# Optimization experiments

Hardware: AMD Instinct MI355X
Metric: run time of the kernel (lower is better)

The kernel has to match this reference:

```python
import jax, jax.numpy as jnp
import numpy as np

B, N, D, S, ITERS = 64, 2048, 256, 8, 3
SCALE = D ** -0.5
EPS_LN = 1e-5

def _ln(x, g, b):
    m = jnp.mean(x, axis=-1, keepdims=True)
    v = jnp.var(x, axis=-1, keepdims=True)
    return (x - m) / jnp.sqrt(v + EPS_LN) * g + b

def setup_inputs() -> dict:
    key = jax.random.key(0)
    ks = jax.random.split(key, 20)
    s = D ** -0.5
    f32 = jnp.float32
    return dict(
        x=jax.random.normal(ks[0], (B, N, D), f32),
        noise=jax.random.normal(ks[1], (B, S, D), f32),
        slots_mu=jax.random.normal(ks[2], (1, 1, D), f32),
        slots_sigma=jax.random.normal(ks[3], (1, 1, D), f32),
        Wq=jax.random.normal(ks[4], (D, D), f32) * s, bq=jnp.zeros((D,), f32),
        Wk=jax.random.normal(ks[5], (D, D), f32) * s, bk=jnp.zeros((D,), f32),
        Wv=jax.random.normal(ks[6], (D, D), f32) * s, bv=jnp.zeros((D,), f32),
        W_ih=jax.random.normal(ks[7], (3 * D, D), f32) * s, b_ih=jnp.zeros((3 * D,), f32),
        W_hh=jax.random.normal(ks[8], (3 * D, D), f32) * s, b_hh=jnp.zeros((3 * D,), f32),
        W1=jax.random.normal(ks[9], (D, D), f32) * s, b1=jnp.zeros((D,), f32),
        W2=jax.random.normal(ks[10], (D, D), f32) * s, b2=jnp.zeros((D,), f32),
        g_in=jnp.ones((D,), f32), be_in=jnp.zeros((D,), f32),
        g_sl=jnp.ones((D,), f32), be_sl=jnp.zeros((D,), f32),
        g_ff=jnp.ones((D,), f32), be_ff=jnp.zeros((D,), f32),
    )

def reference(x, noise, slots_mu, slots_sigma, Wq, bq, Wk, bk, Wv, bv,
              W_ih, b_ih, W_hh, b_hh, W1, b1, W2, b2,
              g_in, be_in, g_sl, be_sl, g_ff, be_ff):
    # slot init: mu + softplus(sigma) * noise  -> [B,S,D]
    slots = slots_mu + jax.nn.softplus(slots_sigma) * noise
    xn = _ln(x, g_in, be_in)
    k = xn @ Wk.T + bk  # [B,N,D]
    v = xn @ Wv.T + bv
    for _ in range(ITERS):
        prev = slots
        q = _ln(slots, g_sl, be_sl) @ Wq.T + bq  # [B,S,D]
        logits = jnp.einsum('bsd,bnd->bsn', q, k) * SCALE
        attn = jax.nn.softmax(logits, axis=-1) + 1e-8  # softmax over inputs, as in source
        attn = attn / jnp.sum(attn, axis=-1, keepdims=True)
        updates = jnp.einsum('bsn,bnd->bsd', attn, v)
        # GRUCell(input=updates, hidden=prev); torch gate order r,z,n
        gi = updates @ W_ih.T + b_ih
        gh = prev @ W_hh.T + b_hh
        ir, iz, i_n = jnp.split(gi, 3, axis=-1)
        hr, hz, h_n = jnp.split(gh, 3, axis=-1)
        r = jax.nn.sigmoid(ir + hr)
        z = jax.nn.sigmoid(iz + hz)
        n = jnp.tanh(i_n + r * h_n)
        slots = (1.0 - z) * n + z * prev
        # residual MLP
        h = jax.nn.relu(_ln(slots, g_ff, be_ff) @ W1.T + b1)
        slots = slots + (h @ W2.T + b2)
    return slots
```

## Files before the change

### kernel.cpp

```cpp
#include <hip/hip_runtime.h>
#include <cstddef>


#define BB 64
#define NN 2048
#define DD 256
#define NCH 32
#define CHK 64
#define NITER 3
#define XPITCH 264

typedef unsigned short u16;
typedef unsigned int u32;
typedef _Float16 h2 __attribute__((ext_vector_type(2)));
typedef _Float16 h4 __attribute__((ext_vector_type(4)));

#if defined(__has_builtin)
#if __has_builtin(__builtin_amdgcn_fdot2)
#define HAS_FDOT2 1
#endif
#endif

#ifdef HAS_FDOT2
#define FDOT2(a,b,c) __builtin_amdgcn_fdot2((a),(b),(c),false)
#else
#define FDOT2(a,b,c) fmaf((float)(a).y,(float)(b).y, fmaf((float)(a).x,(float)(b).x,(c)))
#endif

__device__ __forceinline__ h2 u2h2(u32 v){ union{u32 u; h2 h;} c; c.u=v; return c.h; }
__device__ __forceinline__ float u16f(u16 v){ union{u16 u; _Float16 h;} c; c.u=v; return (float)c.h; }
__device__ __forceinline__ u32 packh2(float a, float b){
  union{u32 u; h2 h;} c; c.h.x=(_Float16)a; c.h.y=(_Float16)b; return c.u;
}

__global__ __launch_bounds__(256) void kA(const float* __restrict__ noise, const float* __restrict__ mu,
                                          const float* __restrict__ sig, float* __restrict__ S,
                                          const float* __restrict__ Wq, const float* __restrict__ Wk,
                                          const float* __restrict__ bq, const float* __restrict__ Wih,
                                          const float* __restrict__ Wv, const float* __restrict__ bv,
                                          const float* __restrict__ bih,
                                          float* __restrict__ Wqk, float* __restrict__ bqk,
                                          float* __restrict__ Wihv, float* __restrict__ bihv){
  __shared__ float col[256];
  const int t = threadIdx.x;
  const int blk = blockIdx.x;
  if(blk < 256){
    col[t] = Wq[t*256 + blk];
    __syncthreads();
    float acc = 0.f;
    #pragma unroll 4
    for(int j=0;j<256;j++) acc += col[j]*Wk[j*256+t];
    Wqk[blk*256+t] = acc * 0.0625f;
  } else if(blk < 1024){
    int c = blk - 256;
    col[t] = Wih[c*256+t];
    __syncthreads();
    float acc = 0.f;
    #pragma unroll 4
    for(int j=0;j<256;j++) acc += col[j]*Wv[j*256+t];
    Wihv[(size_t)c*256+t] = acc;
  } else if(blk < 1536){
    int i = (blk-1024)*256 + t;
    float sg = sig[t];
    float sp = fmaxf(sg, 0.f) + log1pf(expf(-fabsf(sg)));
    S[i] = mu[t] + sp * noise[i];
  } else if(blk == 1536){
    float acc = 0.f;
    for(int j=0;j<256;j++) acc += bq[j]*Wk[j*256+t];
    bqk[t] = acc * 0.0625f;
  } else {
    for(int c=t;c<768;c+=256){
      float acc = 0.f;
      for(int j=0;j<256;j++) acc += Wih[c*256+j]*bv[j];
      bihv[c] = acc + bih[c];
    }
  }
}

__global__ __launch_bounds__(256) void kB(const float* __restrict__ Wihv, const float* __restrict__ Whh,
                                          const float* __restrict__ W1, const float* __restrict__ W2,
                                          float* __restrict__ WihvT, float* __restrict__ WhhT,
                                          float* __restrict__ W1T, float* __restrict__ W2T,
                                          const float* __restrict__ S0, const float* __restrict__ g_sl,
                                          const float* __restrict__ be_sl, const float* __restrict__ Wqk,
                                          const float* __restrict__ bqk, u16* __restrict__ Qh){
  __shared__ float tile[64][65];
  __shared__ float lnA[8][256];
  const int blk = blockIdx.x, t = threadIdx.x;
  if(blk < 128){
    const float* src; float* dst; int R, C, tb;
    if(blk < 48){ src=Wihv; dst=WihvT; R=768; C=256; tb=blk; }
    else if(blk < 96){ src=Whh; dst=WhhT; R=768; C=256; tb=blk-48; }
    else if(blk < 112){ src=W1; dst=W1T; R=256; C=256; tb=blk-96; }
    else { src=W2; dst=W2T; R=256; C=256; tb=blk-112; }
    const int tilesC = C/64;
    const int r0 = (tb/tilesC)*64, c0 = (tb%tilesC)*64;
    const int x = t&63, y = t>>6;
    #pragma unroll
    for(int k=0;k<16;k++) tile[y*16+k][x] = src[(size_t)(r0+y*16+k)*C + c0+x];
    __syncthreads();
    #pragma unroll
    for(int k=0;k<16;k++) dst[(size_t)(c0+y*16+k)*R + r0+x] = tile[x][y*16+k];
    return;
  }
  const int w = t>>6, l = t&63;
  const int r0 = (blk-128)*8;
  #pragma unroll
  for(int rr=0; rr<2; rr++){
    int r = w*2 + rr;
    float4 v = *(const float4*)(S0 + (size_t)(r0+r)*256 + l*4);
    float s1 = v.x+v.y+v.z+v.w;
    float s2 = v.x*v.x+v.y*v.y+v.z*v.z+v.w*v.w;
    #pragma unroll
    for(int off=1; off<64; off<<=1){ s1 += __shfl_xor(s1,off); s2 += __shfl_xor(s2,off); }
    float m = s1*(1.f/256.f);
    float var = s2*(1.f/256.f) - m*m;
    float rs = rsqrtf(var + 1e-5f);
    float4 gg = *(const float4*)(g_sl + l*4);
    float4 bb = *(const float4*)(be_sl + l*4);
    float4 o;
    o.x=(v.x-m)*rs*gg.x+bb.x; o.y=(v.y-m)*rs*gg.y+bb.y;
    o.z=(v.z-m)*rs*gg.z+bb.z; o.w=(v.w-m)*rs*gg.w+bb.w;
    *(float4*)(&lnA[r][l*4]) = o;
  }
  __syncthreads();
  const int c4 = l*4;
  float acc[2][4] = {};
  #pragma unroll 2
  for(int k=0;k<256;k++){
    float4 wv = *(const float4*)(Wqk + (size_t)k*256 + c4);
    float a0 = lnA[2*w][k], a1 = lnA[2*w+1][k];
    acc[0][0]+=a0*wv.x; acc[0][1]+=a0*wv.y; acc[0][2]+=a0*wv.z; acc[0][3]+=a0*wv.w;
    acc[1][0]+=a1*wv.x; acc[1][1]+=a1*wv.y; acc[1][2]+=a1*wv.z; acc[1][3]+=a1*wv.w;
  }
  float4 bq4 = *(const float4*)(bqk + c4);
  #pragma unroll
  for(int rr=0; rr<2; rr++){
    uint2 o;
    o.x = packh2(acc[rr][0]+bq4.x, acc[rr][1]+bq4.y);
    o.y = packh2(acc[rr][2]+bq4.z, acc[rr][3]+bq4.w);
    *(uint2*)(Qh + (size_t)(r0+2*w+rr)*256 + l*4) = o;
  }
}

template<int ITER0>
__global__ __launch_bounds__(512) void k_attnP(const float* __restrict__ x, const float* __restrict__ g_in,
                                               const float* __restrict__ be_in, u16* __restrict__ xn,
                                               const u16* __restrict__ Qh,
                                               float* __restrict__ mP, float* __restrict__ lP,
                                               u16* __restrict__ aPh){
  __shared__ __align__(16) u16 xs[CHK*XPITCH];
  __shared__ h2 qs[8][128];
  __shared__ float plT[8][64];
  __shared__ float mS[8], lS[8];
  const int c = blockIdx.x, b = blockIdx.y, t = threadIdx.x;
  const int w = t>>6, l = t&63;

  if(ITER0){
    const size_t rowbase = (size_t)b*NN + (size_t)c*CHK;
    const float* xb = x + rowbase*DD;
    float4 gg = *(const float4*)(g_in + l*4);
    float4 bb = *(const float4*)(be_in + l*4);
    #pragma unroll
    for(int k=0;k<8;k++){
      int row = w + 8*k;
      float4 v = *(const float4*)(xb + (size_t)row*256 + l*4);
      float s1 = v.x+v.y+v.z+v.w;
      float s2 = v.x*v.x + v.y*v.y + v.z*v.z + v.w*v.w;
      #pragma unroll
      for(int off=1; off<64; off<<=1){ s1 += __shfl_xor(s1,off); s2 += __shfl_xor(s2,off); }
      float m = s1*(1.f/256.f);
      float var = s2*(1.f/256.f) - m*m;
      float rs = rsqrtf(var + 1e-5f);
      uint2 pk;
      pk.x = packh2((v.x-m)*rs*gg.x + bb.x, (v.y-m)*rs*gg.y + bb.y);
      pk.y = packh2((v.z-m)*rs*gg.z + bb.z, (v.w-m)*rs*gg.w + bb.w);
      *(uint2*)(xs + (size_t)row*XPITCH + l*4) = pk;
      *(uint2*)(xn + (rowbase+row)*DD + l*4) = pk;
    }
  } else {
    const uint4* xg4 = (const uint4*)(xn + ((size_t)b*NN + (size_t)c*CHK)*DD);
    #pragma unroll
    for(int k=0;k<4;k++){
      int idx = t + 512*k;
      int n = idx>>5, j = idx&31;
      *(uint4*)(xs + (size_t)n*XPITCH + j*8) = xg4[idx];
    }
  }
  {
    int s = t>>6, pp = t&63;
    uint2 v = *(const uint2*)(Qh + (size_t)(b*8+s)*256 + pp*4);
    *(uint2*)(&qs[s][pp*2]) = v;
  }
  __syncthreads();

  float lg = 0.f;
  {
    const u16* xr = xs + (size_t)l*XPITCH;
    #pragma unroll 4
    for(int d8=0; d8<32; ++d8){
      uint4 u = *(const uint4*)(xr + d8*8);
      h2 xa=u2h2(u.x), xb2=u2h2(u.y), xc=u2h2(u.z), xd=u2h2(u.w);
      const h2* qp = &qs[w][d8*4];
      lg = FDOT2(xa, qp[0], lg);
      lg = FDOT2(xb2, qp[1], lg);
      lg = FDOT2(xc, qp[2], lg);
      lg = FDOT2(xd, qp[3], lg);
    }
  }
  float mx = lg;
  #pragma unroll
  for(int off=1; off<64; off<<=1) mx = fmaxf(mx, __shfl_xor(mx, off));
  float p = __expf(lg - mx);
  float sm = p;
  #pragma unroll
  for(int off=1; off<64; off<<=1) sm += __shfl_xor(sm, off);
  plT[w][l] = p;
  if(l==0){ mS[w] = mx; lS[w] = sm; }
  __syncthreads();

  const size_t pb = (size_t)(b*NCH + c)*8;
  {
    float4 a4 = {0.f,0.f,0.f,0.f};
    const u16* xq = xs + 4*l;
    #pragma unroll 8
    for(int nn=0; nn<CHK; ++nn){
      uint2 u = *(const uint2*)(xq + (size_t)nn*XPITCH);
      h2 ha=u2h2(u.x), hb=u2h2(u.y);
      float pp = plT[w][nn];
      a4.x += pp*(float)ha.x; a4.y += pp*(float)ha.y;
      a4.z += pp*(float)hb.x; a4.w += pp*(float)hb.y;
    }
    uint2 pk;
    pk.x = packh2(a4.x, a4.y);
    pk.y = packh2(a4.z, a4.w);
    *(uint2*)(aPh + (pb + w)*256 + l*4) = pk;
  }
  if(t<8){ mP[pb+t] = mS[t]; lP[pb+t] = lS[t]; }
}

union PostU {
  float Gt[2][4][768];
  struct { float Row[4][256]; float Ht[4][256]; float Lq[4][256]; } m;
};

__global__ __launch_bounds__(512) void k_post(const float* __restrict__ mP, const float* __restrict__ lP,
                                              const u16* __restrict__ aPh, const float* __restrict__ WihvT,
                                              const float* __restrict__ bihv, const float* __restrict__ WhhT,
                                              const float* __restrict__ bhh, const float* __restrict__ Sc,
                                              const float* __restrict__ g_ff, const float* __restrict__ be_ff,
                                              const float* __restrict__ W1T, const float* __restrict__ b1,
                                              const float* __restrict__ W2T, const float* __restrict__ b2,
                                              const float* __restrict__ g_sl, const float* __restrict__ be_sl,
                                              const float* __restrict__ Wqk, const float* __restrict__ bqk,
                                              float* __restrict__ Sout, u16* __restrict__ Qh, int writeQ){
  __shared__ float Ut[4][256];
  __shared__ float Sp[4][256];
  __shared__ float Hp[2][4][256];
  __shared__ PostU uu;
  __shared__ float red2[4][2];
  const int t = threadIdx.x;
  const int r0 = blockIdx.x*4;
  const int b = r0>>3;
  const int w = t>>6, l = t&63;
  const int c = t&255, hh = t>>8;

  #pragma unroll
  for(int k=0;k<2;k++){
    int idx = t + 512*k;
    int r = idx>>8, cc = idx&255;
    int rr = r0 + r, ss = rr&7;
    const float* mpb = mP + b*(NCH*8) + ss;
    const float* lpb = lP + b*(NCH*8) + ss;
    float M = -1e30f;
    #pragma unroll 8
    for(int c8=0;c8<NCH;c8++) M = fmaxf(M, mpb[c8*8]);
    float L = 0.f, u = 0.f;
    size_t base = ((size_t)b*(NCH*8) + ss)*256 + cc;
    #pragma unroll 8
    for(int c8=0;c8<NCH;c8++){
      float wgt = __expf(mpb[c8*8] - M);
      L += lpb[c8*8]*wgt;
      u += wgt*u16f(aPh[base + (size_t)c8*2048]);
    }
    Ut[r][cc] = u/L;
    Sp[r][cc] = Sc[(size_t)rr*256 + cc];
  }
  __syncthreads();

  if(t < 384){
    const int mat = t/192, q4 = (t - mat*192)*4;
    const float* WT = mat ? WhhT : WihvT;
    const float* bb2 = mat ? bhh : bihv;
    const float (*A)[256] = mat ? Sp : Ut;
    float4 bias4 = *(const float4*)(bb2 + q4);
    float4 ac0 = bias4, ac1 = bias4, ac2 = bias4, ac3 = bias4;
    const float* wp = WT + q4;
    #pragma unroll 4
    for(int d=0; d<256; ++d){
      float4 wv = *(const float4*)(wp + (size_t)d*768);
      float a0=A[0][d], a1=A[1][d], a2=A[2][d], a3=A[3][d];
      ac0.x += a0*wv.x; ac0.y += a0*wv.y; ac0.z += a0*wv.z; ac0.w += a0*wv.w;
      ac1.x += a1*wv.x; ac1.y += a1*wv.y; ac1.z += a1*wv.z; ac1.w += a1*wv.w;
      ac2.x += a2*wv.x; ac2.y += a2*wv.y; ac2.z += a2*wv.z; ac2.w += a2*wv.w;
      ac3.x += a3*wv.x; ac3.y += a3*wv.y; ac3.z += a3*wv.z; ac3.w += a3*wv.w;
    }
    *(float4*)(&uu.Gt[mat][0][q4]) = ac0;
    *(float4*)(&uu.Gt[mat][1][q4]) = ac1;
    *(float4*)(&uu.Gt[mat][2][q4]) = ac2;
    *(float4*)(&uu.Gt[mat][3][q4]) = ac3;
  }
  __syncthreads();

  #pragma unroll
  for(int k=0;k<2;k++){
    int idx = t + 512*k;
    int r = idx>>8, cc = idx&255;
    float gir = uu.Gt[0][r][cc], giz = uu.Gt[0][r][256+cc], gin = uu.Gt[0][r][512+cc];
    float ghr = uu.Gt[1][r][cc], ghz = uu.Gt[1][r][256+cc], ghn = uu.Gt[1][r][512+cc];
    float rr2 = 1.f/(1.f + __expf(-(gir+ghr)));
    float zz = 1.f/(1.f + __expf(-(giz+ghz)));
    float nn = tanhf(gin + rr2*ghn);
    Ut[r][cc] = (1.f-zz)*nn + zz*Sp[r][cc];
  }
  __syncthreads();

  if(w < 4){
    float s1=0.f, s2=0.f;
    #pragma unroll
    for(int k2=0;k2<4;k2++){ float v = Ut[w][l + 64*k2]; s1 += v; s2 += v*v; }
    #pragma unroll
    for(int off=1; off<64; off<<=1){ s1 += __shfl_xor(s1,off); s2 += __shfl_xor(s2,off); }
    if(l==0){
      float m = s1*(1.f/256.f);
      float var = s2*(1.f/256.f) - m*m;
      red2[w][0] = m; red2[w][1] = rsqrtf(var + 1e-5f);
    }
  }
  __syncthreads();
  #pragma unroll
  for(int k=0;k<2;k++){
    int idx = t + 512*k;
    int r = idx>>8, cc = idx&255;
    uu.m.Row[r][cc] = (Ut[r][cc]-red2[r][0])*red2[r][1]*g_ff[cc] + be_ff[cc];
  }
  __syncthreads();

  {
    const float* w1 = W1T + (size_t)hh*128*256 + c;
    float a0 = hh ? 0.f : b1[c], a1=a0, a2=a0, a3=a0;
    const int dB = hh*128;
    #pragma unroll 8
    for(int d=0; d<128; ++d){
      float wv = w1[(size_t)d*256];
      a0 += uu.m.Row[0][dB+d]*wv;
      a1 += uu.m.Row[1][dB+d]*wv;
      a2 += uu.m.Row[2][dB+d]*wv;
      a3 += uu.m.Row[3][dB+d]*wv;
    }
    Hp[hh][0][c]=a0; Hp[hh][1][c]=a1; Hp[hh][2][c]=a2; Hp[hh][3][c]=a3;
  }
  __syncthreads();
  #pragma unroll
  for(int k=0;k<2;k++){
    int idx = t + 512*k;
    int r = idx>>8, cc = idx&255;
    uu.m.Ht[r][cc] = fmaxf(Hp[0][r][cc]+Hp[1][r][cc], 0.f);
  }
  __syncthreads();

  {
    const float* w2 = W2T + (size_t)hh*128*256 + c;
    float a0 = hh ? 0.f : b2[c], a1=a0, a2=a0, a3=a0;
    const int dB = hh*128;
    #pragma unroll 8
    for(int d=0; d<128; ++d){
      float wv = w2[(size_t)d*256];
      a0 += uu.m.Ht[0][dB+d]*wv;
      a1 += uu.m.Ht[1][dB+d]*wv;
      a2 += uu.m.Ht[2][dB+d]*wv;
      a3 += uu.m.Ht[3][dB+d]*wv;
    }
    Hp[hh][0][c]=a0; Hp[hh][1][c]=a1; Hp[hh][2][c]=a2; Hp[hh][3][c]=a3;
  }
  __syncthreads();
  if(t < 256){
    #pragma unroll
    for(int r=0;r<4;r++){
      float sn = Hp[0][r][c] + Hp[1][r][c] + Ut[r][c];
      Sout[(size_t)(r0+r)*256 + c] = sn;
      Ut[r][c] = sn;
    }
  }

  if(writeQ){
    __syncthreads();
    if(w < 4){
      float s1=0.f, s2=0.f;
      #pragma unroll
      for(int k2=0;k2<4;k2++){ float v = Ut[w][l + 64*k2]; s1 += v; s2 += v*v; }
      #pragma unroll
      for(int off=1; off<64; off<<=1){ s1 += __shfl_xor(s1,off); s2 += __shfl_xor(s2,off); }
      if(l==0){
        float m = s1*(1.f/256.f);
        float var = s2*(1.f/256.f) - m*m;
        red2[w][0] = m; red2[w][1] = rsqrtf(var + 1e-5f);
      }
    }
    __syncthreads();
    #pragma unroll
    for(int k=0;k<2;k++){
      int idx = t + 512*k;
      int r = idx>>8, cc = idx&255;
      uu.m.Lq[r][cc] = (Ut[r][cc]-red2[r][0])*red2[r][1]*g_sl[cc] + be_sl[cc];
    }
    __syncthreads();
    {
      const float* wq = Wqk + (size_t)hh*128*256 + c;
      float a0 = hh ? 0.f : bqk[c], a1=a0, a2=a0, a3=a0;
      const int dB = hh*128;
      #pragma unroll 8
      for(int d=0; d<128; ++d){
        float wv = wq[(size_t)d*256];
        a0 += uu.m.Lq[0][dB+d]*wv;
        a1 += uu.m.Lq[1][dB+d]*wv;
        a2 += uu.m.Lq[2][dB+d]*wv;
        a3 += uu.m.Lq[3][dB+d]*wv;
      }
      Hp[hh][0][c]=a0; Hp[hh][1][c]=a1; Hp[hh][2][c]=a2; Hp[hh][3][c]=a3;
    }
    __syncthreads();
    if(t < 256){
      #pragma unroll
      for(int r=0;r<4;r++)
        uu.m.Row[r][c] = Hp[0][r][c] + Hp[1][r][c];
    }
    __syncthreads();
    {
      int r = t>>7, pp = t&127;
      u32 v = packh2(uu.m.Row[r][2*pp], uu.m.Row[r][2*pp+1]);
      *(u32*)(Qh + (size_t)(r0+r)*256 + pp*2) = v;
    }
  }
}

extern "C" void kernel_launch(void* const* d_in, const int* in_sizes, int n_in,
                              void* d_out, int out_size, void* d_ws, size_t ws_size,
                              hipStream_t stream){
  const float* x    = (const float*)d_in[0];
  const float* noise= (const float*)d_in[1];
  const float* mu   = (const float*)d_in[2];
  const float* sig  = (const float*)d_in[3];
  const float* Wq   = (const float*)d_in[4];
  const float* bq   = (const float*)d_in[5];
  const float* Wk   = (const float*)d_in[6];
  const float* Wv   = (const float*)d_in[8];
  const float* bv   = (const float*)d_in[9];
  const float* W_ih = (const float*)d_in[10];
  const float* b_ih = (const float*)d_in[11];
  const float* W_hh = (const float*)d_in[12];
  const float* b_hh = (const float*)d_in[13];
  const float* W1m  = (const float*)d_in[14];
  const float* b1v  = (const float*)d_in[15];
  const float* W2m  = (const float*)d_in[16];
  const float* b2v  = (const float*)d_in[17];
  const float* g_in = (const float*)d_in[18];
  const float* be_in= (const float*)d_in[19];
  const float* g_sl = (const float*)d_in[20];
  const float* be_sl= (const float*)d_in[21];
  const float* g_ff = (const float*)d_in[22];
  const float* be_ff= (const float*)d_in[23];

  char* p = (char*)d_ws;
  auto alloc = [&](size_t bytes)->char*{ char* q = p; p += (bytes + 255) & ~(size_t)255; return q; };
  u16*   xn    = (u16*)  alloc((size_t)BB*NN*DD*2);
  float* Wqk   = (float*)alloc(256*256*4);
  float* bqk   = (float*)alloc(256*4);
  float* Wihv  = (float*)alloc((size_t)768*256*4);
  float* WihvT = (float*)alloc((size_t)256*768*4);
  float* bihv  = (float*)alloc(768*4);
  float* WhhT  = (float*)alloc((size_t)256*768*4);
  float* W1T   = (float*)alloc(256*256*4);
  float* W2T   = (float*)alloc(256*256*4);
  float* S0    = (float*)alloc(512*256*4);
  float* S1    = (float*)alloc(512*256*4);
  u16*   Qh    = (u16*)  alloc(512*256*2);
  float* mP    = (float*)alloc(64*NCH*8*4);
  float* lP    = (float*)alloc(64*NCH*8*4);
  u16*   aPh   = (u16*)  alloc((size_t)64*NCH*8*256*2);
  if((size_t)(p - (char*)d_ws) > ws_size) return;

  kA<<<1538, 256, 0, stream>>>(noise, mu, sig, S0, Wq, Wk, bq, W_ih, Wv, bv, b_ih,
                               Wqk, bqk, Wihv, bihv);
  kB<<<192, 256, 0, stream>>>(Wihv, W_hh, W1m, W2m, WihvT, WhhT, W1T, W2T,
                              S0, g_sl, be_sl, Wqk, bqk, Qh);

  float* Sin = S0;
  float* Sping[2] = { S1, S0 };
  for(int it=0; it<NITER; ++it){
    float* Sout = (it==NITER-1) ? (float*)d_out : Sping[it&1];
    if(it == 0)
      k_attnP<1><<<dim3(NCH, 64), 512, 0, stream>>>(x, g_in, be_in, xn, Qh, mP, lP, aPh);
    else
      k_attnP<0><<<dim3(NCH, 64), 512, 0, stream>>>(x, g_in, be_in, xn, Qh, mP, lP, aPh);
    k_post<<<128, 512, 0, stream>>>(mP, lP, aPh, WihvT, bihv, WhhT, b_hh, Sin, g_ff, be_ff,
                                    W1T, b1v, W2T, b2v, g_sl, be_sl, Wqk, bqk,
                                    Sout, Qh, (it<NITER-1) ? 1 : 0);
    Sin = Sout;
  }
}
```

Before: 328.3 us.

## Swizzle attention LDS tile and load chunks directly into LDS

Replaces the padded-pitch LDS layout for the x-chunk tile with an unpadded XOR-swizzled layout. On non-first iterations it fills that tile with global_load_lds when the builtin is available, bypassing registers. It also swaps the grid dimensions so consecutive blocks walk batches rather than chunks. The goal is fewer LDS bank conflicts and less load overhead. The direct-to-LDS path relies on per-wave contiguous LDS placement matching the swizzle, which is easy to get wrong.

Measured after the change: 336.0 us. 2.4% more time.

```diff
diff --git a/kernel.cpp b/kernel.cpp
--- a/kernel.cpp
+++ b/kernel.cpp
@@ -8,7 +8,6 @@
 #define NCH 32
 #define CHK 64
 #define NITER 3
-#define XPITCH 264
 
 typedef unsigned short u16;
 typedef unsigned int u32;
@@ -18,6 +17,9 @@
 #if defined(__has_builtin)
 #if __has_builtin(__builtin_amdgcn_fdot2)
 #define HAS_FDOT2 1
+#endif
+#if __has_builtin(__builtin_amdgcn_global_load_lds)
+#define HAS_GLL 1
 #endif
 #endif
 
@@ -149,11 +151,12 @@
                                                const u16* __restrict__ Qh,
                                                float* __restrict__ mP, float* __restrict__ lP,
                                                u16* __restrict__ aPh){
-  __shared__ __align__(16) u16 xs[CHK*XPITCH];
+  __shared__ __align__(16) u16 xs[CHK*256];
   __shared__ h2 qs[8][128];
   __shared__ float plT[8][64];
   __shared__ float mS[8], lS[8];
-  const int c = blockIdx.x, b = blockIdx.y, t = threadIdx.x;
+  char* xsb = (char*)xs;
+  const int b = blockIdx.x, c = blockIdx.y, t = threadIdx.x;
   const int w = t>>6, l = t&63;
 
   if(ITER0){
@@ -175,17 +178,32 @@
       uint2 pk;
       pk.x = packh2((v.x-m)*rs*gg.x + bb.x, (v.y-m)*rs*gg.y + bb.y);
       pk.y = packh2((v.z-m)*rs*gg.z + bb.z, (v.w-m)*rs*gg.w + bb.w);
-      *(uint2*)(xs + (size_t)row*XPITCH + l*4) = pk;
+      *(uint2*)(xsb + (size_t)row*512 + (((l>>1)^(row&31))<<4) + (l&1)*8) = pk;
       *(uint2*)(xn + (rowbase+row)*DD + l*4) = pk;
     }
   } else {
+#ifdef HAS_GLL
+    const char* gb = (const char*)(xn + ((size_t)b*NN + (size_t)c*CHK)*DD);
+    #pragma unroll
+    for(int k=0;k<4;k++){
+      int slot = w*4 + k;
+      int row = 2*slot + (l>>5);
+      int jlog = (l&31) ^ (row&31);
+      const void* gp = gb + (size_t)row*512 + ((size_t)jlog<<4);
+      void* lp = (void*)(xsb + (size_t)slot*1024);
+      __builtin_amdgcn_global_load_lds((const __attribute__((address_space(1))) void*)gp,
+                                       (__attribute__((address_space(3))) void*)lp, 16, 0, 0);
+    }
+#else
     const uint4* xg4 = (const uint4*)(xn + ((size_t)b*NN + (size_t)c*CHK)*DD);
     #pragma unroll
     for(int k=0;k<4;k++){
       int idx = t + 512*k;
-      int n = idx>>5, j = idx&31;
-      *(uint4*)(xs + (size_t)n*XPITCH + j*8) = xg4[idx];
-    }
+      int row = idx>>5, jlog = idx&31;
+      uint4 v = xg4[idx];
+      *(uint4*)(xsb + (size_t)row*512 + (((size_t)(jlog^(row&31)))<<4)) = v;
+    }
+#endif
   }
   {
     int s = t>>6, pp = t&63;
@@ -196,12 +214,13 @@
 
   float lg = 0.f;
   {
-    const u16* xr = xs + (size_t)l*XPITCH;
+    const char* xr = xsb + (size_t)l*512;
+    const int swz = l & 31;
     #pragma unroll 4
-    for(int d8=0; d8<32; ++d8){
-      uint4 u = *(const uint4*)(xr + d8*8);
+    for(int jl=0; jl<32; ++jl){
+      uint4 u = *(const uint4*)(xr + ((size_t)(jl^swz)<<4));
       h2 xa=u2h2(u.x), xb2=u2h2(u.y), xc=u2h2(u.z), xd=u2h2(u.w);
-      const h2* qp = &qs[w][d8*4];
+      const h2* qp = &qs[w][jl*4];
       lg = FDOT2(xa, qp[0], lg);
       lg = FDOT2(xb2, qp[1], lg);
       lg = FDOT2(xc, qp[2], lg);
@@ -222,10 +241,10 @@
   const size_t pb = (size_t)(b*NCH + c)*8;
   {
     float4 a4 = {0.f,0.f,0.f,0.f};
-    const u16* xq = xs + 4*l;
+    const int jq = l>>1, half = (l&1)*8;
     #pragma unroll 8
     for(int nn=0; nn<CHK; ++nn){
-      uint2 u = *(const uint2*)(xq + (size_t)nn*XPITCH);
+      uint2 u = *(const uint2*)(xsb + (size_t)nn*512 + (((size_t)(jq^(nn&31)))<<4) + half);
       h2 ha=u2h2(u.x), hb=u2h2(u.y);
       float pp = plT[w][nn];
       a4.x += pp*(float)ha.x; a4.y += pp*(float)ha.y;
@@ -500,9 +519,9 @@
   for(int it=0; it<NITER; ++it){
     float* Sout = (it==NITER-1) ? (float*)d_out : Sping[it&1];
     if(it == 0)
-      k_attnP<1><<<dim3(NCH, 64), 512, 0, stream>>>(x, g_in, be_in, xn, Qh, mP, lP, aPh);
+      k_attnP<1><<<dim3(64, NCH), 512, 0, stream>>>(x, g_in, be_in, xn, Qh, mP, lP, aPh);
     else
-      k_attnP<0><<<dim3(NCH, 64), 512, 0, stream>>>(x, g_in, be_in, xn, Qh, mP, lP, aPh);
+      k_attnP<0><<<dim3(64, NCH), 512, 0, stream>>>(x, g_in, be_in, xn, Qh, mP, lP, aPh);
     k_post<<<128, 512, 0, stream>>>(mP, lP, aPh, WihvT, bihv, WhhT, b_hh, Sin, g_ff, be_ff,
                                     W1T, b1v, W2T, b2v, g_sl, be_sl, Wqk, bqk,
                                     Sout, Qh, (it<NITER-1) ? 1 : 0);
```
